# Kernel tuning notes

Hardware: AMD Instinct MI355X
Metric: run time of the kernel (lower is better)

The kernel has to match this reference:

```python
import jax, jax.numpy as jnp
import numpy as np
from jax.scipy.special import logsumexp

B, N, F_IN, HID = 8, 1024, 256, 128
RATIO = 0.5
NUM_LAYERS = 2
EPS_OT = 0.01  # forward default epsilon


def setup_inputs():
    key = jax.random.key(0)
    ks = jax.random.split(key, 6)
    x = jax.random.normal(ks[0], (B, N, F_IN), dtype=jnp.float32)
    adj = (jax.random.uniform(ks[1], (B, N, N)) < 0.02).astype(jnp.float32)
    adj = jnp.maximum(adj, jnp.swapaxes(adj, 1, 2))  # symmetric sparse-ish graph
    mask = jnp.ones((B, N), dtype=bool)
    W1 = jax.random.normal(ks[2], (F_IN, HID), dtype=jnp.float32) / np.sqrt(F_IN)
    b1 = jnp.zeros((HID,), dtype=jnp.float32)
    Watt = jax.random.normal(ks[3], (HID, 1), dtype=jnp.float32) / np.sqrt(HID)
    batt = jnp.zeros((1,), dtype=jnp.float32)
    W2 = jax.random.normal(ks[4], (HID, F_IN), dtype=jnp.float32) / np.sqrt(HID)
    b2 = jnp.zeros((F_IN,), dtype=jnp.float32)
    return dict(x=x, adj=adj, mask=mask, W1=W1, b1=b1, Watt=Watt, batt=batt,
                W2=W2, b2=b2, opt_epochs=20)


def _gcn_norm(adj):
    # DenseGCNConv add_loop + symmetric normalization
    n = adj.shape[-1]
    A = adj + jnp.eye(n, dtype=adj.dtype)
    d = jnp.maximum(A.sum(-1), 1.0) ** -0.5
    return d[..., :, None] * A * d[..., None, :]


def dense_gcn(x, adj, W, b, mask=None):
    out = jnp.einsum('bij,bjh->bih', _gcn_norm(adj), x @ W) + b
    if mask is not None:
        out = out * mask[..., None].astype(out.dtype)
    return out


def normalize_batch_adj(adj):
    # CoarsenBlock.normalize_batch_adj: self-loop sym-norm, zero-row masked
    n = adj.shape[-1]
    A = adj + jnp.eye(n, dtype=adj.dtype)
    d = jnp.maximum(A.sum(-1), 1.0) ** -0.5
    newA = d[..., :, None] * A * d[..., None, :]
    return (adj.sum(-1) > 0).astype(adj.dtype)[..., None] * newA


def coarsen_block(x, adj, Watt, batt):
    # attention score per node, squared then sigmoid  -> [B, N]
    alpha = jax.nn.sigmoid(dense_gcn(x, adj, Watt, batt) ** 2)[..., 0]
    norm_adj = normalize_batch_adj(adj)
    k = int(adj.shape[1] * RATIO) + 1
    cut = jax.lax.top_k(alpha, k)[0][:, -1]                 # per-sample k-th value
    cut_alpha = jax.nn.relu(alpha + 1e-7 - cut[:, None])    # soft top-k gate
    S = norm_adj * cut_alpha[:, None, :]
    S = S / jnp.maximum(jnp.abs(S).sum(-1, keepdims=True), 1e-12)  # row L1 norm
    emb = jnp.einsum('bij,bif->bjf', S, x)                  # S^T x
    tmp = jnp.einsum('bij,bik->bjk', S, adj)                # S^T adj
    new_adj = jnp.einsum('bjk,bkl->bjl', tmp, S)            # S^T adj S
    return emb, new_adj, S


def sinkhorn_loss(x, y, eps, niter):
    # squared-euclidean cost via gram trick (no [n,m,f] intermediate)
    C = (jnp.sum(x * x, -1)[:, None] + jnp.sum(y * y, -1)[None, :]
         - 2.0 * (x @ y.T))
    n, m = C.shape
    log_mu = jnp.full((n,), -np.log(n), dtype=C.dtype)
    log_nu = jnp.full((m,), -np.log(m), dtype=C.dtype)

    def M(u, v):
        return (-C + u[:, None] + v[None, :]) / eps

    def step(carry, _):
        u, v = carry
        u = eps * (log_mu - logsumexp(M(u, v), axis=1)) + u
        v = eps * (log_nu - logsumexp(M(u, v), axis=0)) + v
        return (u, v), None

    (u, v), _ = jax.lax.scan(step, (jnp.zeros_like(log_mu), jnp.zeros_like(log_nu)),
                             None, length=niter)
    pi = jnp.exp(M(u, v))
    return jnp.sum(pi * C)


def reference(x, adj, mask, W1, b1, Watt, batt, W2, b2, opt_epochs):
    x1 = jax.nn.relu(dense_gcn(x, adj, W1, b1, mask))
    xs0 = x1.mean(axis=1)
    new_adjs = [adj]
    Ss = []
    coarse_x, new_adj = x1, adj
    for _ in range(NUM_LAYERS):
        coarse_x, new_adj, S = coarsen_block(coarse_x, new_adj, Watt, batt)
        new_adjs.append(new_adj)
        Ss.append(S)
    x2 = dense_gcn(coarse_x, new_adj, W2, b2, mask)
    xs1 = x2.mean(axis=1)
    loss_fn = lambda a, b: sinkhorn_loss(a, b, EPS_OT, opt_epochs)
    opt_loss = jnp.sum(jax.vmap(loss_fn)(x, x2))
    return (xs0, xs1, new_adjs[0], new_adjs[1], new_adjs[2], Ss[0], Ss[1], opt_loss)
```

## Files before the change

kernel.cpp:

```cpp
#include <hip/hip_runtime.h>
#include <math.h>

#define BN   8
#define NN   1024
#define FIN  256
#define HIDN 128
#define KTOP 513
#define NITER 20
#define EPS_S 0.01f
#define INV_EPS 100.0f
#define LOG_MU (-6.9314718055994531f)
#define SNB 256

typedef __attribute__((ext_vector_type(8))) short bfrag8;
typedef __attribute__((ext_vector_type(4))) float facc4;

#define GLOAD16(g, l) __builtin_amdgcn_global_load_lds( \
    (const __attribute__((address_space(1))) unsigned int*)(g), \
    (__attribute__((address_space(3))) unsigned int*)(l), 16, 0, 0)

static __device__ __forceinline__ float wred_sum(float s) {
#pragma unroll
  for (int o = 32; o > 0; o >>= 1) s += __shfl_xor(s, o);
  return s;
}
static __device__ __forceinline__ unsigned short f2b(float f) {
  unsigned int u = __float_as_uint(f);
  u += 0x7fff + ((u >> 16) & 1);
  return (unsigned short)(u >> 16);
}
static __device__ __forceinline__ float b2f(unsigned short h) {
  return __uint_as_float((unsigned int)h << 16);
}

template<int WRBF, int WCOPY>
__global__ __launch_bounds__(256) void k_rowstats4(const float* __restrict__ adj,
                                                   float* __restrict__ dv,
                                                   float* __restrict__ rm,
                                                   unsigned short* __restrict__ abf,
                                                   float* __restrict__ ocopy) {
  int r0 = blockIdx.x << 2;
  int t = threadIdx.x, lane = t & 63, wv = t >> 6;
  __shared__ float sm[4][4];
#pragma unroll
  for (int r = 0; r < 4; ++r) {
    float4 v = ((const float4*)(adj + (long)(r0 + r) * NN))[t];
    if (WRBF) {
      ushort4 h; h.x = f2b(v.x); h.y = f2b(v.y); h.z = f2b(v.z); h.w = f2b(v.w);
      *(ushort4*)(abf + (long)(r0 + r) * NN + t * 4) = h;
    }
    if (WCOPY) ((float4*)(ocopy + (long)(r0 + r) * NN))[t] = v;
    float s = (v.x + v.y) + (v.z + v.w);
    s = wred_sum(s);
    if (lane == 0) sm[wv][r] = s;
  }
  __syncthreads();
  if (t < 4) {
    float tot = sm[0][t] + sm[1][t] + sm[2][t] + sm[3][t];
    dv[r0 + t] = rsqrtf(fmaxf(tot + 1.0f, 1.0f));
    rm[r0 + t] = tot > 0.0f ? 1.0f : 0.0f;
  }
}

__global__ __launch_bounds__(256) void k_f2b(const float* __restrict__ X,
                                             unsigned short* __restrict__ Y) {
  long i = ((long)blockIdx.x * 256 + threadIdx.x) * 4;
  float4 v = *(const float4*)(X + i);
  Y[i] = f2b(v.x); Y[i + 1] = f2b(v.y); Y[i + 2] = f2b(v.z); Y[i + 3] = f2b(v.w);
}

__global__ __launch_bounds__(256) void k_w1t(const float* __restrict__ W,
                                             unsigned short* __restrict__ Wt) {
  int idx = blockIdx.x * 256 + threadIdx.x;
  int n = idx >> 8, k = idx & 255;
  Wt[idx] = f2b(W[k * HIDN + n]);
}

__global__ __launch_bounds__(256) void k_split2(const float* __restrict__ X,
                                                unsigned short* __restrict__ Xh,
                                                unsigned short* __restrict__ Xl) {
  long i = ((long)blockIdx.x * 256 + threadIdx.x) * 4;
  float4 v = *(const float4*)(X + i);
  ushort4 h, l;
  h.x = f2b(v.x); l.x = f2b(v.x - b2f(h.x));
  h.y = f2b(v.y); l.y = f2b(v.y - b2f(h.y));
  h.z = f2b(v.z); l.z = f2b(v.z - b2f(h.z));
  h.w = f2b(v.w); l.w = f2b(v.w - b2f(h.w));
  *(ushort4*)(Xh + i) = h;
  *(ushort4*)(Xl + i) = l;
}

__global__ __launch_bounds__(256) void k_transp(const float* __restrict__ X,
                                                unsigned short* __restrict__ Xt,
                                                int R, int C) {
  __shared__ float tile[64][65];
  long bb = blockIdx.z;
  const float* Xb = X + bb * (long)R * C;
  unsigned short* Xtb = Xt + bb * (long)R * C;
  int r0 = blockIdx.y * 64, c0 = blockIdx.x * 64;
  int t = threadIdx.x;
  int tr = t >> 4, tc4 = (t & 15) * 4;
#pragma unroll
  for (int p = 0; p < 4; ++p) {
    float4 v = *(const float4*)(Xb + (long)(r0 + tr + p * 16) * C + c0 + tc4);
    tile[tr + p * 16][tc4 + 0] = v.x; tile[tr + p * 16][tc4 + 1] = v.y;
    tile[tr + p * 16][tc4 + 2] = v.z; tile[tr + p * 16][tc4 + 3] = v.w;
  }
  __syncthreads();
  int jj = t >> 2, i0 = (t & 3) * 16;
  unsigned short* orow = Xtb + (long)(c0 + jj) * R + r0 + i0;
#pragma unroll
  for (int q = 0; q < 16; ++q) orow[q] = f2b(tile[i0 + q][jj]);
}

template<int SPLIT>
__global__ __launch_bounds__(256) void k_stc(const float* __restrict__ XW,
                                             const float* __restrict__ dvv,
                                             unsigned short* __restrict__ Bh,
                                             unsigned short* __restrict__ Bl,
                                             int F) {
  __shared__ float tile[64][65];
  __shared__ float dl[64];
  int bz = blockIdx.z;
  const float* Xb = XW + (long)bz * NN * F;
  int j0 = blockIdx.x * 64;
  int n0 = blockIdx.y * 64;
  int t = threadIdx.x;
  int tr = t >> 4, tc4 = (t & 15) * 4;
#pragma unroll
  for (int p = 0; p < 4; ++p) {
    float4 v = *(const float4*)(Xb + (long)(j0 + tr + p * 16) * F + n0 + tc4);
    tile[tr + p * 16][tc4 + 0] = v.x; tile[tr + p * 16][tc4 + 1] = v.y;
    tile[tr + p * 16][tc4 + 2] = v.z; tile[tr + p * 16][tc4 + 3] = v.w;
  }
  if (t < 64) dl[t] = dvv[(bz << 10) + j0 + t];
  __syncthreads();
  int nn = t >> 2, i0 = (t & 3) * 16;
  long obase = ((long)bz * F + n0 + nn) * NN + j0 + i0;
#pragma unroll
  for (int q = 0; q < 16; ++q) {
    float v = tile[i0 + q][nn] * dl[i0 + q];
    unsigned short h = f2b(v);
    Bh[obase + q] = h;
    if (SPLIT) Bl[obase + q] = f2b(v - b2f(h));
  }
}

template<int WF32, int WBF>
__global__ __launch_bounds__(256) void k_mfma_nt(
    const unsigned short* __restrict__ A, const unsigned short* __restrict__ B,
    float* __restrict__ Cf, unsigned short* __restrict__ Cb,
    unsigned short* __restrict__ Cb2,
    int K, int ldA, int ldB, int ldC, long sA, long sB, long sC) {
  __shared__ unsigned short As[128 * 32];
  __shared__ unsigned short Bs[128 * 32];
  int bz = blockIdx.z;
  A += bz * sA; B += bz * sB;
  int m0 = blockIdx.y * 128, n0 = blockIdx.x * 128;
  int tid = threadIdx.x, lane = tid & 63, w = tid >> 6;
  int wr = w >> 1, wc = w & 1;
  facc4 acc[4][4];
#pragma unroll
  for (int i = 0; i < 4; ++i)
#pragma unroll
    for (int j = 0; j < 4; ++j)
#pragma unroll
      for (int q = 0; q < 4; ++q) acc[i][j][q] = 0.f;

  int rA0 = w * 16 + (lane >> 2);
  int kslot = lane & 3;

  for (int k0 = 0; k0 < K; k0 += 32) {
#pragma unroll
    for (int i = 0; i < 2; ++i) {
      int row = i * 64 + rA0;
      int ks = (kslot ^ (row & 3)) << 3;
      GLOAD16(A + (long)(m0 + row) * ldA + k0 + ks, As + (i * 64 + w * 16) * 32);
      GLOAD16(B + (long)(n0 + row) * ldB + k0 + ks, Bs + (i * 64 + w * 16) * 32);
    }
    __syncthreads();
    bfrag8 af[4], bfr[4];
#pragma unroll
    for (int mi = 0; mi < 4; ++mi) {
      int row = wr * 64 + mi * 16 + (lane & 15);
      int sl = (((lane >> 4) ^ (row & 3)) << 3);
      af[mi] = *(const bfrag8*)(As + row * 32 + sl);
    }
#pragma unroll
    for (int ni = 0; ni < 4; ++ni) {
      int row = wc * 64 + ni * 16 + (lane & 15);
      int sl = (((lane >> 4) ^ (row & 3)) << 3);
      bfr[ni] = *(const bfrag8*)(Bs + row * 32 + sl);
    }
#pragma unroll
    for (int mi = 0; mi < 4; ++mi)
#pragma unroll
      for (int ni = 0; ni < 4; ++ni)
        acc[mi][ni] = __builtin_amdgcn_mfma_f32_16x16x32_bf16(
            af[mi], bfr[ni], acc[mi][ni], 0, 0, 0);
    __syncthreads();
  }
  if (WF32) Cf += bz * sC;
  if (WBF) Cb += bz * sC;
  if (WBF == 2) Cb2 += bz * sC;
#pragma unroll
  for (int mi = 0; mi < 4; ++mi) {
    int rowb = m0 + wr * 64 + mi * 16 + ((lane >> 4) << 2);
#pragma unroll
    for (int ni = 0; ni < 4; ++ni) {
      int col = n0 + wc * 64 + ni * 16 + (lane & 15);
#pragma unroll
      for (int q = 0; q < 4; ++q) {
        long off = (long)(rowb + q) * ldC + col;
        float v = acc[mi][ni][q];
        if (WF32) Cf[off] = v;
        if (WBF == 1) Cb[off] = f2b(v);
        if (WBF == 2) {
          unsigned short h = f2b(v);
          Cb[off] = h;
          Cb2[off] = f2b(v - b2f(h));
        }
      }
    }
  }
}

template<int SPLIT, int RELU>
__global__ __launch_bounds__(256) void k_mfma_gcn(
    const unsigned short* __restrict__ Ah, const unsigned short* __restrict__ Al,
    const unsigned short* __restrict__ Bh, const unsigned short* __restrict__ Bl,
    const float* __restrict__ dvv, const float* __restrict__ XW,
    const float* __restrict__ bias, float* __restrict__ Cf, int F) {
  __shared__ unsigned short AsH[128 * 32], BsH[128 * 32];
  __shared__ unsigned short AsL[SPLIT ? 128 * 32 : 16], BsL[SPLIT ? 128 * 32 : 16];
  int bz = blockIdx.z;
  const unsigned short* Ahb = Ah + (long)bz * NN * NN;
  const unsigned short* Alb = SPLIT ? Al + (long)bz * NN * NN : nullptr;
  const unsigned short* Bhb = Bh + (long)bz * F * NN;
  const unsigned short* Blb = SPLIT ? Bl + (long)bz * F * NN : nullptr;
  int m0 = blockIdx.y * 128, n0 = blockIdx.x * 128;
  int tid = threadIdx.x, lane = tid & 63, w = tid >> 6;
  int wr = w >> 1, wc = w & 1;
  facc4 acc[4][4];
#pragma unroll
  for (int i = 0; i < 4; ++i)
#pragma unroll
    for (int j = 0; j < 4; ++j)
#pragma unroll
      for (int q = 0; q < 4; ++q) acc[i][j][q] = 0.f;

  int rA0 = w * 16 + (lane >> 2);
  int kslot = lane & 3;

  for (int k0 = 0; k0 < NN; k0 += 32) {
#pragma unroll
    for (int i = 0; i < 2; ++i) {
      int row = i * 64 + rA0;
      int ks = (kslot ^ (row & 3)) << 3;
      int ld = (i * 64 + w * 16) * 32;
      GLOAD16(Ahb + (long)(m0 + row) * NN + k0 + ks, AsH + ld);
      GLOAD16(Bhb + (long)(n0 + row) * NN + k0 + ks, BsH + ld);
      if (SPLIT) {
        GLOAD16(Alb + (long)(m0 + row) * NN + k0 + ks, AsL + ld);
        GLOAD16(Blb + (long)(n0 + row) * NN + k0 + ks, BsL + ld);
      }
    }
    __syncthreads();
    bfrag8 afh[4], bfh[4], afl[4], bfl[4];
#pragma unroll
    for (int mi = 0; mi < 4; ++mi) {
      int row = wr * 64 + mi * 16 + (lane & 15);
      int sl = (((lane >> 4) ^ (row & 3)) << 3);
      afh[mi] = *(const bfrag8*)(AsH + row * 32 + sl);
      if (SPLIT) afl[mi] = *(const bfrag8*)(AsL + row * 32 + sl);
    }
#pragma unroll
    for (int ni = 0; ni < 4; ++ni) {
      int row = wc * 64 + ni * 16 + (lane & 15);
      int sl = (((lane >> 4) ^ (row & 3)) << 3);
      bfh[ni] = *(const bfrag8*)(BsH + row * 32 + sl);
      if (SPLIT) bfl[ni] = *(const bfrag8*)(BsL + row * 32 + sl);
    }
#pragma unroll
    for (int mi = 0; mi < 4; ++mi)
#pragma unroll
      for (int ni = 0; ni < 4; ++ni) {
        acc[mi][ni] = __builtin_amdgcn_mfma_f32_16x16x32_bf16(
            afh[mi], bfh[ni], acc[mi][ni], 0, 0, 0);
        if (SPLIT) {
          acc[mi][ni] = __builtin_amdgcn_mfma_f32_16x16x32_bf16(
              afh[mi], bfl[ni], acc[mi][ni], 0, 0, 0);
          acc[mi][ni] = __builtin_amdgcn_mfma_f32_16x16x32_bf16(
              afl[mi], bfh[ni], acc[mi][ni], 0, 0, 0);
        }
      }
    __syncthreads();
  }
  Cf += (long)bz * NN * F;
#pragma unroll
  for (int mi = 0; mi < 4; ++mi) {
    int rowb = m0 + wr * 64 + mi * 16 + ((lane >> 4) << 2);
#pragma unroll
    for (int ni = 0; ni < 4; ++ni) {
      int col = n0 + wc * 64 + ni * 16 + (lane & 15);
      float bcol = bias[col];
#pragma unroll
      for (int q = 0; q < 4; ++q) {
        float dm = dvv[(bz << 10) + rowb + q];
        float xwv = XW[((long)(bz << 10) + rowb + q) * F + col];
        float v = dm * (acc[mi][ni][q] + dm * xwv) + bcol;
        if (RELU) v = fmaxf(v, 0.f);
        Cf[(long)(rowb + q) * F + col] = v;
      }
    }
  }
}

__global__ __launch_bounds__(256) void k_mfma_gram(
    const unsigned short* __restrict__ Ah, const unsigned short* __restrict__ Al,
    const unsigned short* __restrict__ Bh, const unsigned short* __restrict__ Bl,
    const float* __restrict__ xx, const float* __restrict__ yy,
    float* __restrict__ Cf, float* __restrict__ Ct) {
  __shared__ unsigned short AsH[128 * 32], AsL[128 * 32];
  __shared__ unsigned short BsH[128 * 32], BsL[128 * 32];
  int bz = blockIdx.z;
  long boff = (long)bz * NN * FIN;
  Ah += boff; Al += boff; Bh += boff; Bl += boff;
  const float* xxb = xx + (bz << 10);
  const float* yyb = yy + (bz << 10);
  int m0 = blockIdx.y * 128, n0 = blockIdx.x * 128;
  int tid = threadIdx.x, lane = tid & 63, w = tid >> 6;
  int wr = w >> 1, wc = w & 1;
  facc4 acc[4][4];
#pragma unroll
  for (int i = 0; i < 4; ++i)
#pragma unroll
    for (int j = 0; j < 4; ++j)
#pragma unroll
      for (int q = 0; q < 4; ++q) acc[i][j][q] = 0.f;

  int rA0 = w * 16 + (lane >> 2);
  int kslot = lane & 3;

  for (int k0 = 0; k0 < FIN; k0 += 32) {
#pragma unroll
    for (int i = 0; i < 2; ++i) {
      int row = i * 64 + rA0;
      int ks = (kslot ^ (row & 3)) << 3;
      long ga = (long)(m0 + row) * FIN + k0 + ks;
      long gb = (long)(n0 + row) * FIN + k0 + ks;
      int ld = (i * 64 + w * 16) * 32;
      GLOAD16(Ah + ga, AsH + ld);
      GLOAD16(Al + ga, AsL + ld);
      GLOAD16(Bh + gb, BsH + ld);
      GLOAD16(Bl + gb, BsL + ld);
    }
    __syncthreads();
    bfrag8 afh[4], afl[4], bfh[4], bfl[4];
#pragma unroll
    for (int mi = 0; mi < 4; ++mi) {
      int row = wr * 64 + mi * 16 + (lane & 15);
      int sl = (((lane >> 4) ^ (row & 3)) << 3);
      afh[mi] = *(const bfrag8*)(AsH + row * 32 + sl);
      afl[mi] = *(const bfrag8*)(AsL + row * 32 + sl);
    }
#pragma unroll
    for (int ni = 0; ni < 4; ++ni) {
      int row = wc * 64 + ni * 16 + (lane & 15);
      int sl = (((lane >> 4) ^ (row & 3)) << 3);
      bfh[ni] = *(const bfrag8*)(BsH + row * 32 + sl);
      bfl[ni] = *(const bfrag8*)(BsL + row * 32 + sl);
    }
#pragma unroll
    for (int mi = 0; mi < 4; ++mi)
#pragma unroll
      for (int ni = 0; ni < 4; ++ni) {
        acc[mi][ni] = __builtin_amdgcn_mfma_f32_16x16x32_bf16(
            afh[mi], bfh[ni], acc[mi][ni], 0, 0, 0);
        acc[mi][ni] = __builtin_amdgcn_mfma_f32_16x16x32_bf16(
            afh[mi], bfl[ni], acc[mi][ni], 0, 0, 0);
        acc[mi][ni] = __builtin_amdgcn_mfma_f32_16x16x32_bf16(
            afl[mi], bfh[ni], acc[mi][ni], 0, 0, 0);
      }
    __syncthreads();
  }
  Cf += (long)bz * NN * NN;
  Ct += (long)bz * NN * NN;
#pragma unroll
  for (int mi = 0; mi < 4; ++mi) {
    int rowb = m0 + wr * 64 + mi * 16 + ((lane >> 4) << 2);
#pragma unroll
    for (int ni = 0; ni < 4; ++ni) {
      int col = n0 + wc * 64 + ni * 16 + (lane & 15);
      float yv = yyb[col];
      float4 tv;
#pragma unroll
      for (int q = 0; q < 4; ++q) {
        float v = xxb[rowb + q] + yv - 2.f * acc[mi][ni][q];
        Cf[(long)(rowb + q) * NN + col] = v;
        ((float*)&tv)[q] = v;
      }
      *(float4*)(Ct + (long)col * NN + rowb) = tv;
    }
  }
}

__global__ __launch_bounds__(256) void k_rowdot(const float* __restrict__ X,
                                                const float* __restrict__ w,
                                                float* __restrict__ out) {
  int t = threadIdx.x; int lane = t & 63; int wv = t >> 6;
  int row = blockIdx.x * 4 + wv;
  const float* xr = X + (long)row * HIDN;
  float s = xr[lane] * w[lane] + xr[lane + 64] * w[lane + 64];
  s = wred_sum(s);
  if (lane == 0) out[row] = s;
}

__global__ __launch_bounds__(256) void k_alpha4(const float* __restrict__ adj,
                                                const float* __restrict__ dv,
                                                const float* __restrict__ s0,
                                                const float* __restrict__ batt,
                                                float* __restrict__ alpha) {
  int r0 = blockIdx.x << 2; int b = r0 >> 10; int i0 = r0 & (NN - 1);
  int t = threadIdx.x, lane = t & 63, wv = t >> 6;
  float4 d4 = ((const float4*)(dv + (b << 10)))[t];
  float4 s4 = ((const float4*)(s0 + (b << 10)))[t];
  float w4[4];
  w4[0] = d4.x * s4.x; w4[1] = d4.y * s4.y; w4[2] = d4.z * s4.z; w4[3] = d4.w * s4.w;
  __shared__ float sm[4][4];
#pragma unroll
  for (int r = 0; r < 4; ++r) {
    float4 a4 = ((const float4*)(adj + (long)(r0 + r) * NN))[t];
    float dot = a4.x * w4[0] + a4.y * w4[1] + a4.z * w4[2] + a4.w * w4[3];
    int i = i0 + r;
    if ((i >> 2) == t) dot += w4[i & 3];
    dot = wred_sum(dot);
    if (lane == 0) sm[wv][r] = dot;
  }
  __syncthreads();
  if (t < 4) {
    float dot = sm[0][t] + sm[1][t] + sm[2][t] + sm[3][t];
    float tt = dv[r0 + t] * dot + batt[0];
    alpha[r0 + t] = 1.f / (1.f + __expf(-tt * tt));
  }
}

__global__ __launch_bounds__(512) void k_topk(const float* __restrict__ alpha,
                                              float* __restrict__ cut) {
  __shared__ float smv[NN];
  int b = blockIdx.x; int t = threadIdx.x;
  smv[t] = alpha[(b << 10) + t];
  smv[t + 512] = alpha[(b << 10) + t + 512];
  __syncthreads();
  for (int k2 = 2; k2 <= NN; k2 <<= 1) {
    for (int j2 = k2 >> 1; j2 > 0; j2 >>= 1) {
      int i = ((t / j2) * (j2 << 1)) + (t % j2);
      int ixj = i + j2;
      bool up = ((i & k2) == 0);
      float a = smv[i], c = smv[ixj];
      if ((a > c) == up) { smv[i] = c; smv[ixj] = a; }
      __syncthreads();
    }
  }
  if (t == 0) cut[b] = smv[NN - KTOP];
}

__global__ __launch_bounds__(256) void k_sbuild4(const float* __restrict__ adj,
                                                 const float* __restrict__ dv,
                                                 const float* __restrict__ rm,
                                                 const float* __restrict__ alpha,
                                                 const float* __restrict__ cut,
                                                 float* __restrict__ S) {
  int r0 = blockIdx.x << 2; int b = r0 >> 10; int i0 = r0 & (NN - 1);
  int t = threadIdx.x, lane = t & 63, wv = t >> 6;
  float cb = cut[b];
  float4 d4 = ((const float4*)(dv + (b << 10)))[t];
  float4 al4 = ((const float4*)(alpha + (b << 10)))[t];
  float4 dg;
  dg.x = d4.x * fmaxf(al4.x + 1e-7f - cb, 0.f);
  dg.y = d4.y * fmaxf(al4.y + 1e-7f - cb, 0.f);
  dg.z = d4.z * fmaxf(al4.z + 1e-7f - cb, 0.f);
  dg.w = d4.w * fmaxf(al4.w + 1e-7f - cb, 0.f);
  __shared__ float sm[4][4];
  __shared__ float sinv[4];
  float4 vals[4];
#pragma unroll
  for (int r = 0; r < 4; ++r) {
    float di = dv[r0 + r] * rm[r0 + r];
    float4 a4 = ((const float4*)(adj + (long)(r0 + r) * NN))[t];
    int i = i0 + r;
    if ((i >> 2) == t) ((float*)&a4)[i & 3] += 1.f;
    vals[r].x = di * dg.x * a4.x; vals[r].y = di * dg.y * a4.y;
    vals[r].z = di * dg.z * a4.z; vals[r].w = di * dg.w * a4.w;
    float s = (fabsf(vals[r].x) + fabsf(vals[r].y)) +
              (fabsf(vals[r].z) + fabsf(vals[r].w));
    s = wred_sum(s);
    if (lane == 0) sm[wv][r] = s;
  }
  __syncthreads();
  if (t < 4) sinv[t] = 1.f / fmaxf(sm[0][t] + sm[1][t] + sm[2][t] + sm[3][t], 1e-12f);
  __syncthreads();
#pragma unroll
  for (int r = 0; r < 4; ++r) {
    float inv = sinv[r];
    float4 o; o.x = vals[r].x * inv; o.y = vals[r].y * inv;
    o.z = vals[r].z * inv; o.w = vals[r].w * inv;
    ((float4*)(S + (long)(r0 + r) * NN))[t] = o;
  }
}

template<int GCN>
__global__ __launch_bounds__(256) void k_gemm_ks(
    const float* __restrict__ A, const float* __restrict__ Bm, float* __restrict__ P,
    int M, int Nn, int K, int KS, long sA, long sB,
    const float* __restrict__ dv) {
  __shared__ float As[8][132];
  __shared__ float Bs[8][132];
  int z = blockIdx.z;
  int b = z / KS, ks = z % KS;
  int KC = K / KS;
  A += (long)b * sA; Bm += (long)b * sB;
  const float* dvb = GCN ? (dv + (long)b * NN) : nullptr;
  int m0 = blockIdx.y * 128, n0 = blockIdx.x * 128;
  int tid = threadIdx.x;
  int tx = tid & 15, ty = tid >> 4;
  float acc[8][8];
#pragma unroll
  for (int i = 0; i < 8; i++)
#pragma unroll
    for (int j = 0; j < 8; j++) acc[i][j] = 0.f;

  float drow = 0.f;
  if (GCN) drow = dvb[m0 + (tid >> 1)];

  for (int k0 = ks * KC; k0 < ks * KC + KC; k0 += 8) {
    {
      int r = tid >> 1, c4 = (tid & 1) * 4;
      float4 av = *(const float4*)(A + (long)(m0 + r) * K + k0 + c4);
      float a4[4] = {av.x, av.y, av.z, av.w};
      if (GCN) {
#pragma unroll
        for (int q = 0; q < 4; ++q) {
          int gj = k0 + c4 + q;
          float val = a4[q] + ((m0 + r) == gj ? 1.f : 0.f);
          a4[q] = drow * dvb[gj] * val;
        }
      }
      As[c4 + 0][r] = a4[0]; As[c4 + 1][r] = a4[1];
      As[c4 + 2][r] = a4[2]; As[c4 + 3][r] = a4[3];
    }
    {
      int kr = tid >> 5, c4 = (tid & 31) * 4;
      float4 bv = *(const float4*)(Bm + (long)(k0 + kr) * Nn + n0 + c4);
      *(float4*)&Bs[kr][c4] = bv;
    }
    __syncthreads();
#pragma unroll
    for (int k = 0; k < 8; ++k) {
      float av[8], bv[8];
      *(float4*)&av[0] = *(const float4*)&As[k][ty * 8];
      *(float4*)&av[4] = *(const float4*)&As[k][ty * 8 + 4];
      *(float4*)&bv[0] = *(const float4*)&Bs[k][tx * 8];
      *(float4*)&bv[4] = *(const float4*)&Bs[k][tx * 8 + 4];
#pragma unroll
      for (int i = 0; i < 8; i++)
#pragma unroll
        for (int j = 0; j < 8; j++)
          acc[i][j] = fmaf(av[i], bv[j], acc[i][j]);
    }
    __syncthreads();
  }
  float* Pz = P + (long)z * M * Nn;
#pragma unroll
  for (int i = 0; i < 8; ++i) {
    int m = m0 + ty * 8 + i;
    float* prow = Pz + (long)m * Nn + n0 + tx * 8;
    *(float4*)&prow[0] = *(float4*)&acc[i][0];
    *(float4*)&prow[4] = *(float4*)&acc[i][4];
  }
}

template<int RELU, int BIAS>
__global__ __launch_bounds__(256) void k_red_bias(
    const float* __restrict__ P, const float* __restrict__ bias,
    float* __restrict__ out, int Nn, int KS, long chunk) {
  long u = ((long)blockIdx.x * 256 + threadIdx.x) * 4;
  long b = u / chunk; long rem = u % chunk;
  const float* p = P + b * KS * chunk + rem;
  float4 s = *(const float4*)p;
  for (int k = 1; k < KS; ++k) {
    float4 q = *(const float4*)(p + (long)k * chunk);
    s.x += q.x; s.y += q.y; s.z += q.z; s.w += q.w;
  }
  if (BIAS) {
    int n = (int)(rem % Nn);
    s.x += bias[n]; s.y += bias[n + 1]; s.z += bias[n + 2]; s.w += bias[n + 3];
  }
  if (RELU) {
    s.x = fmaxf(s.x, 0.f); s.y = fmaxf(s.y, 0.f);
    s.z = fmaxf(s.z, 0.f); s.w = fmaxf(s.w, 0.f);
  }
  *(float4*)(out + u) = s;
}

__global__ __launch_bounds__(256) void k_colmean(const float* __restrict__ X, int Fd,
                                                 float* __restrict__ out) {
  int nb = Fd >> 6;
  int b = blockIdx.x / nb; int f0 = (blockIdx.x % nb) << 6;
  int t = threadIdx.x;
  int f = f0 + (t & 63); int rc = t >> 6;
  const float* xb = X + (long)b * NN * Fd;
  float s = 0.f;
  for (int i = rc * 256; i < rc * 256 + 256; ++i) s += xb[(long)i * Fd + f];
  __shared__ float sm[256];
  sm[t] = s; __syncthreads();
  if (t < 64) out[b * Fd + f] = (sm[t] + sm[t + 64] + sm[t + 128] + sm[t + 192]) * (1.f / NN);
}

__global__ __launch_bounds__(256) void k_sqnorm(const float* __restrict__ X, int Fd,
                                                float* __restrict__ out) {
  int t = threadIdx.x; int lane = t & 63; int wv = t >> 6;
  int row = blockIdx.x * 4 + wv;
  const float* xr = X + (long)row * Fd;
  float s = 0.f;
  for (int f = lane; f < Fd; f += 64) { float v = xr[f]; s = fmaf(v, v, s); }
  s = wred_sum(s);
  if (lane == 0) out[row] = s;
}


static __device__ __forceinline__ float4 load_cohere4(const float* p) {
  float4 v;
  asm volatile("global_load_dwordx4 %0, %1, off sc0 sc1\n\ts_waitcnt vmcnt(0)"
               : "=v"(v) : "v"(p) : "memory");
  return v;
}
static __device__ __forceinline__ float load_cohere1(const float* p) {
  float v;
  asm volatile("global_load_dword %0, %1, off sc0 sc1\n\ts_waitcnt vmcnt(0)"
               : "=v"(v) : "v"(p) : "memory");
  return v;
}
static __device__ __forceinline__ void store_cohere1(float* p, float v) {
  asm volatile("global_store_dword %0, %1, off sc0 sc1\n\ts_waitcnt vmcnt(0)"
               :: "v"(p), "v"(v) : "memory");
}

static __device__ __forceinline__ void stage_vec(float* __restrict__ vls,
                                                 const float* __restrict__ src,
                                                 int t) {
  if (t < 256) {
    float4 v = load_cohere4(src + t * 4);
    *(float4*)(vls + t * 4) = v;
  }
  __syncthreads();
}

static __device__ __forceinline__ void group_bar(int* __restrict__ slots,
                                                 int bid, int grp, int t, int g1) {
  __syncthreads();
  if (t == 0)
    __hip_atomic_store(&slots[bid * 16], g1, __ATOMIC_RELAXED,
                       __HIP_MEMORY_SCOPE_AGENT);
  if (t < 32) {
    int idx = ((grp << 5) + t) * 16;
    int spin = 0;
    while (__hip_atomic_load(&slots[idx], __ATOMIC_RELAXED,
                             __HIP_MEMORY_SCOPE_AGENT) < g1) {
      if (++spin > (1 << 20)) break;
      __builtin_amdgcn_s_sleep(1);
    }
  }
  __syncthreads();
}

template<int LOSS>
static __device__ __forceinline__ void pass_reg(const float4 (&Cr)[16],
    const float* __restrict__ vls, float* __restrict__ uout,
    int jc, int row, float* __restrict__ lossacc) {
  float mx = -3.0e38f;
#pragma unroll
  for (int k = 0; k < 16; ++k) {
    float4 v4 = *(const float4*)(vls + (k * 16 + jc) * 4);
    float ax = v4.x - Cr[k].x, ay = v4.y - Cr[k].y;
    float az = v4.z - Cr[k].z, aw = v4.w - Cr[k].w;
    mx = fmaxf(mx, fmaxf(fmaxf(ax, ay), fmaxf(az, aw)));
  }
#pragma unroll
  for (int m = 1; m <= 8; m <<= 1) mx = fmaxf(mx, __shfl_xor(mx, m));
  float ls = 0.f, ld = 0.f;
#pragma unroll
  for (int k = 0; k < 16; ++k) {
    float4 v4 = *(const float4*)(vls + (k * 16 + jc) * 4);
    float e;
    e = __expf(v4.x - Cr[k].x - mx); ls += e; if (LOSS) ld = fmaf(e, Cr[k].x, ld);
    e = __expf(v4.y - Cr[k].y - mx); ls += e; if (LOSS) ld = fmaf(e, Cr[k].y, ld);
    e = __expf(v4.z - Cr[k].z - mx); ls += e; if (LOSS) ld = fmaf(e, Cr[k].z, ld);
    e = __expf(v4.w - Cr[k].w - mx); ls += e; if (LOSS) ld = fmaf(e, Cr[k].w, ld);
  }
#pragma unroll
  for (int m = 1; m <= 8; m <<= 1) {
    ls += __shfl_xor(ls, m);
    if (LOSS) ld += __shfl_xor(ld, m);
  }
  if (jc == 0) {
    float uval = LOG_MU - (mx + __logf(ls));
    store_cohere1(uout + row, uval);
    if (LOSS) *lossacc += (ld / ls) * (1.0f / 1024.0f);
  }
}

__global__ __launch_bounds__(512, 2) void k_sink_reg(
    const float* __restrict__ Cm, const float* __restrict__ Ct,
    float* __restrict__ uvv, float* __restrict__ vvv,
    float* __restrict__ part, float* __restrict__ oloss,
    int* __restrict__ slots1, int* __restrict__ slots2) {
  int bid = blockIdx.x, t = threadIdx.x, lane = t & 63, wvi = t >> 6;
  int jc = lane & 15;
  int row = bid * 32 + wvi * 4 + (lane >> 4);
  int b = bid >> 5;
  __shared__ float vls[1024];
  float4 Creg[16], Ctreg[16];
  {
    const float4* cp = (const float4*)(Cm + (long)row * NN);
    const float4* tp = (const float4*)(Ct + (long)row * NN);
#pragma unroll
    for (int k = 0; k < 16; ++k) {
      float4 c = cp[k * 16 + jc], ct = tp[k * 16 + jc];
      Creg[k].x = c.x * INV_EPS;  Creg[k].y = c.y * INV_EPS;
      Creg[k].z = c.z * INV_EPS;  Creg[k].w = c.w * INV_EPS;
      Ctreg[k].x = ct.x * INV_EPS; Ctreg[k].y = ct.y * INV_EPS;
      Ctreg[k].z = ct.z * INV_EPS; Ctreg[k].w = ct.w * INV_EPS;
    }
  }
  const float* ub = uvv + (b << 10);
  const float* vb = vvv + (b << 10);
  float lossacc = 0.f;
  int g1 = 1;
  for (int it = 0; it < NITER; ++it) {
    stage_vec(vls, vb, t);
    pass_reg<0>(Creg, vls, uvv, jc, row, nullptr);
    group_bar(slots1, bid, b, t, g1); ++g1;
    stage_vec(vls, ub, t);
    if (it < NITER - 1) {
      pass_reg<0>(Ctreg, vls, vvv, jc, row, nullptr);
      group_bar(slots1, bid, b, t, g1); ++g1;
    } else {
      pass_reg<1>(Ctreg, vls, vvv, jc, row, &lossacc);
    }
  }
  float s = wred_sum(lossacc);
  __shared__ float lsm[8];
  if (lane == 0) lsm[wvi] = s;
  __syncthreads();
  if (t == 0) {
    float ps = 0.f;
#pragma unroll
    for (int i = 0; i < 8; ++i) ps += lsm[i];
    store_cohere1(part + bid, ps);
    __hip_atomic_store(&slots2[bid * 16], 1, __ATOMIC_RELAXED,
                       __HIP_MEMORY_SCOPE_AGENT);
  }
  if (bid == 0) {
    if (t < SNB) {
      int spin = 0;
      while (__hip_atomic_load(&slots2[t * 16], __ATOMIC_RELAXED,
                               __HIP_MEMORY_SCOPE_AGENT) < 1) {
        if (++spin > (1 << 20)) break;
        __builtin_amdgcn_s_sleep(1);
      }
    }
    __syncthreads();
    float s2 = 0.f;
    if (t < SNB) s2 = load_cohere1(part + t);
    s2 = wred_sum(s2);
    __shared__ float sm2[8];
    if (lane == 0) sm2[wvi] = s2;
    __syncthreads();
    if (t == 0) {
      float tot = 0.f;
#pragma unroll
      for (int i = 0; i < 8; ++i) tot += sm2[i];
      oloss[0] = tot * EPS_S;
    }
  }
}

extern "C" void kernel_launch(void* const* d_in, const int* in_sizes, int n_in,
                              void* d_out, int out_size, void* d_ws, size_t ws_size,
                              hipStream_t stream) {
  const float* x    = (const float*)d_in[0];
  const float* adj  = (const float*)d_in[1];
  const float* W1   = (const float*)d_in[3];
  const float* b1   = (const float*)d_in[4];
  const float* Watt = (const float*)d_in[5];
  const float* batt = (const float*)d_in[6];
  const float* W2   = (const float*)d_in[7];
  const float* b2   = (const float*)d_in[8];

  float* out = (float*)d_out;
  float* xs0   = out;
  float* xs1   = out + 1024;
  float* oadj0 = out + 3072;
  float* oadj1 = oadj0 + 8388608;
  float* oadj2 = oadj1 + 8388608;
  float* oS0   = oadj2 + 8388608;
  float* oS1   = oS0 + 8388608;
  float* oloss = oS1 + 8388608;

  float* ws   = (float*)d_ws;
  float* wXW  = ws;
  float* wCXA = wXW + 2097152;
  float* wCXB = wCXA + 1048576;
  float* wR   = wCXB + 1048576;
  float* wX2  = wR + 8388608;
  float* wStf = wX2 + 2097152;
  float* wCxtf= wStf + 4194304;
  float* wCt  = wCxtf + 524288;
  float* smb  = wCt + 8388608;

  unsigned short* tmp_bf = (unsigned short*)wR;
  unsigned short* a2h    = (unsigned short*)wCt;
  unsigned short* a2l    = a2h + 8388608;
  unsigned short* adj_bf = (unsigned short*)oadj2;
  unsigned short* St     = (unsigned short*)wStf;
  unsigned short* cxt    = (unsigned short*)wCxtf;
  unsigned short* x_bf   = (unsigned short*)wStf;
  unsigned short* Bg1    = (unsigned short*)wCxtf;
  unsigned short* Bg2h   = (unsigned short*)wStf;
  unsigned short* Bg2l   = (unsigned short*)(wStf + 2097152);
  unsigned short* xh  = (unsigned short*)wStf;
  unsigned short* xl  = xh + 2097152;
  unsigned short* x2h = xh + 4194304;
  unsigned short* x2l = xh + 6291456;
  float* Cmat = wR;
  float* d0 = smb;            float* rm0 = smb + 8192;
  float* d1 = smb + 16384;    float* rm1 = smb + 24576;
  float* d2 = smb + 32768;    float* rm2 = smb + 40960;
  float* s0v = smb + 49152;   float* alp = smb + 57344;
  float* xxv = smb + 65536;   float* yyv = smb + 73728;
  float* uv  = smb + 81920;   float* vv  = smb + 90112;
  float* cutv = smb + 98304;  float* part = smb + 98368;
  unsigned short* W1t = (unsigned short*)(smb + 98624);
  int* ibar = (int*)(smb + 115008);
  int* slots1 = ibar;
  int* slots2 = ibar + 4096;

  k_rowstats4<1, 1><<<2048, 256, 0, stream>>>(adj, d0, rm0, adj_bf, oadj0);

  k_f2b<<<2048, 256, 0, stream>>>(x, x_bf);
  k_w1t<<<128, 256, 0, stream>>>(W1, W1t);
  k_mfma_nt<1, 0><<<dim3(1, 64, 1), 256, 0, stream>>>(x_bf, W1t, wXW, nullptr,
      nullptr, 256, 256, 256, 128, 0L, 0L, 0L);
  k_stc<0><<<dim3(16, 2, 8), 256, 0, stream>>>(wXW, d0, Bg1, nullptr, HIDN);
  k_mfma_gcn<0, 1><<<dim3(1, 8, 8), 256, 0, stream>>>(adj_bf, nullptr, Bg1,
      nullptr, d0, wXW, b1, wCXA, HIDN);
  k_colmean<<<16, 256, 0, stream>>>(wCXA, HIDN, xs0);

  k_rowdot<<<2048, 256, 0, stream>>>(wCXA, Watt, s0v);
  k_alpha4<<<2048, 256, 0, stream>>>(adj, d0, s0v, batt, alp);
  k_topk<<<8, 512, 0, stream>>>(alp, cutv);
  k_sbuild4<<<2048, 256, 0, stream>>>(adj, d0, rm0, alp, cutv, oS0);
  k_transp<<<dim3(16, 16, 8), 256, 0, stream>>>(oS0, St, 1024, 1024);
  k_transp<<<dim3(2, 16, 8), 256, 0, stream>>>(wCXA, cxt, 1024, 128);
  k_mfma_nt<1, 0><<<dim3(1, 8, 8), 256, 0, stream>>>(St, cxt, wCXB, nullptr,
      nullptr, 1024, 1024, 1024, 128, 1048576L, 131072L, 131072L);
  k_mfma_nt<0, 1><<<dim3(8, 8, 8), 256, 0, stream>>>(St, adj_bf, nullptr, tmp_bf,
      nullptr, 1024, 1024, 1024, 1024, 1048576L, 1048576L, 1048576L);
  k_mfma_nt<1, 1><<<dim3(8, 8, 8), 256, 0, stream>>>(tmp_bf, St, oadj1, adj_bf,
      nullptr, 1024, 1024, 1024, 1024, 1048576L, 1048576L, 1048576L);
  k_rowstats4<0, 0><<<2048, 256, 0, stream>>>(oadj1, d1, rm1, nullptr, nullptr);

  k_rowdot<<<2048, 256, 0, stream>>>(wCXB, Watt, s0v);
  k_alpha4<<<2048, 256, 0, stream>>>(oadj1, d1, s0v, batt, alp);
  k_topk<<<8, 512, 0, stream>>>(alp, cutv);
  k_sbuild4<<<2048, 256, 0, stream>>>(oadj1, d1, rm1, alp, cutv, oS1);
  k_transp<<<dim3(16, 16, 8), 256, 0, stream>>>(oS1, St, 1024, 1024);
  k_transp<<<dim3(2, 16, 8), 256, 0, stream>>>(wCXB, cxt, 1024, 128);
  k_mfma_nt<1, 0><<<dim3(1, 8, 8), 256, 0, stream>>>(St, cxt, wCXA, nullptr,
      nullptr, 1024, 1024, 1024, 128, 1048576L, 131072L, 131072L);
  k_mfma_nt<0, 1><<<dim3(8, 8, 8), 256, 0, stream>>>(St, adj_bf, nullptr, tmp_bf,
      nullptr, 1024, 1024, 1024, 1024, 1048576L, 1048576L, 1048576L);
  k_mfma_nt<1, 2><<<dim3(8, 8, 8), 256, 0, stream>>>(tmp_bf, St, oadj2, a2h,
      a2l, 1024, 1024, 1024, 1024, 1048576L, 1048576L, 1048576L);
  k_rowstats4<0, 0><<<2048, 256, 0, stream>>>(oadj2, d2, rm2, nullptr, nullptr);

  k_gemm_ks<0><<<dim3(2, 64, 2), 256, 0, stream>>>(wCXA, W2, wR, 8192, FIN, HIDN,
      2, 0L, 0L, nullptr);
  k_red_bias<0, 0><<<2048, 256, 0, stream>>>(wR, nullptr, wXW, FIN, 2, 2097152L);
  k_stc<1><<<dim3(16, 4, 8), 256, 0, stream>>>(wXW, d2, Bg2h, Bg2l, FIN);
  k_mfma_gcn<1, 0><<<dim3(2, 8, 8), 256, 0, stream>>>(a2h, a2l, Bg2h, Bg2l,
      d2, wXW, b2, wX2, FIN);
  k_colmean<<<32, 256, 0, stream>>>(wX2, FIN, xs1);

  k_sqnorm<<<2048, 256, 0, stream>>>(x, FIN, xxv);
  k_sqnorm<<<2048, 256, 0, stream>>>(wX2, FIN, yyv);
  k_split2<<<2048, 256, 0, stream>>>(x, xh, xl);
  k_split2<<<2048, 256, 0, stream>>>(wX2, x2h, x2l);
  k_mfma_gram<<<dim3(8, 8, 8), 256, 0, stream>>>(xh, xl, x2h, x2l, xxv, yyv,
      Cmat, wCt);
  hipMemsetAsync(uv, 0, (size_t)2 * 8192 * 4, stream);
  hipMemsetAsync(ibar, 0, (size_t)8192 * 4, stream);
  k_sink_reg<<<SNB, 512, 0, stream>>>(Cmat, wCt, uv, vv, part, oloss,
                                      slots1, slots2);
}
```

Before: 749.3 us.

## Fuse coarsening GEMMs into one launch, fuse split with sqnorm, remap sinkhorn groups

```diff
diff --git a/kernel.cpp b/kernel.cpp
--- a/kernel.cpp
+++ b/kernel.cpp
@@ -76,18 +76,24 @@
   Wt[idx] = f2b(W[k * HIDN + n]);
 }
 
-__global__ __launch_bounds__(256) void k_split2(const float* __restrict__ X,
-                                                unsigned short* __restrict__ Xh,
-                                                unsigned short* __restrict__ Xl) {
-  long i = ((long)blockIdx.x * 256 + threadIdx.x) * 4;
-  float4 v = *(const float4*)(X + i);
+__global__ __launch_bounds__(256) void k_prep(const float* __restrict__ X,
+                                              unsigned short* __restrict__ Xh,
+                                              unsigned short* __restrict__ Xl,
+                                              float* __restrict__ sq) {
+  int t = threadIdx.x, lane = t & 63, wv = t >> 6;
+  int row = blockIdx.x * 4 + wv;
+  long base = (long)row * FIN + lane * 4;
+  float4 v = *(const float4*)(X + base);
   ushort4 h, l;
   h.x = f2b(v.x); l.x = f2b(v.x - b2f(h.x));
   h.y = f2b(v.y); l.y = f2b(v.y - b2f(h.y));
   h.z = f2b(v.z); l.z = f2b(v.z - b2f(h.z));
   h.w = f2b(v.w); l.w = f2b(v.w - b2f(h.w));
-  *(ushort4*)(Xh + i) = h;
-  *(ushort4*)(Xl + i) = l;
+  *(ushort4*)(Xh + base) = h;
+  *(ushort4*)(Xl + base) = l;
+  float s = v.x * v.x + v.y * v.y + v.z * v.z + v.w * v.w;
+  s = wred_sum(s);
+  if (lane == 0) sq[row] = s;
 }
 
 __global__ __launch_bounds__(256) void k_transp(const float* __restrict__ X,
@@ -220,6 +226,80 @@
           Cb[off] = h;
           Cb2[off] = f2b(v - b2f(h));
         }
+      }
+    }
+  }
+}
+
+__global__ __launch_bounds__(256) void k_coars(
+    const unsigned short* __restrict__ St, const unsigned short* __restrict__ Badj,
+    const unsigned short* __restrict__ cxt,
+    unsigned short* __restrict__ tmpo, float* __restrict__ embo) {
+  __shared__ unsigned short As[128 * 32];
+  __shared__ unsigned short Bs[128 * 32];
+  int bz = blockIdx.z;
+  int bx = blockIdx.x;
+  int em = (bx == 8);
+  const unsigned short* A = St + (long)bz * 1048576;
+  const unsigned short* B = em ? (cxt + (long)bz * 131072)
+                               : (Badj + (long)bz * 1048576);
+  int m0 = blockIdx.y * 128, n0 = em ? 0 : bx * 128;
+  int tid = threadIdx.x, lane = tid & 63, w = tid >> 6;
+  int wr = w >> 1, wc = w & 1;
+  facc4 acc[4][4];
+#pragma unroll
+  for (int i = 0; i < 4; ++i)
+#pragma unroll
+    for (int j = 0; j < 4; ++j)
+#pragma unroll
+      for (int q = 0; q < 4; ++q) acc[i][j][q] = 0.f;
+
+  int rA0 = w * 16 + (lane >> 2);
+  int kslot = lane & 3;
+
+  for (int k0 = 0; k0 < NN; k0 += 32) {
+#pragma unroll
+    for (int i = 0; i < 2; ++i) {
+      int row = i * 64 + rA0;
+      int ks = (kslot ^ (row & 3)) << 3;
+      GLOAD16(A + (long)(m0 + row) * NN + k0 + ks, As + (i * 64 + w * 16) * 32);
+      GLOAD16(B + (long)(n0 + row) * NN + k0 + ks, Bs + (i * 64 + w * 16) * 32);
+    }
+    __syncthreads();
+    bfrag8 af[4], bfr[4];
+#pragma unroll
+    for (int mi = 0; mi < 4; ++mi) {
+      int row = wr * 64 + mi * 16 + (lane & 15);
+      int sl = (((lane >> 4) ^ (row & 3)) << 3);
+      af[mi] = *(const bfrag8*)(As + row * 32 + sl);
+    }
+#pragma unroll
+    for (int ni = 0; ni < 4; ++ni) {
+      int row = wc * 64 + ni * 16 + (lane & 15);
+      int sl = (((lane >> 4) ^ (row & 3)) << 3);
+      bfr[ni] = *(const bfrag8*)(Bs + row * 32 + sl);
+    }
+#pragma unroll
+    for (int mi = 0; mi < 4; ++mi)
+#pragma unroll
+      for (int ni = 0; ni < 4; ++ni)
+        acc[mi][ni] = __builtin_amdgcn_mfma_f32_16x16x32_bf16(
+            af[mi], bfr[ni], acc[mi][ni], 0, 0, 0);
+    __syncthreads();
+  }
+#pragma unroll
+  for (int mi = 0; mi < 4; ++mi) {
+    int rowb = m0 + wr * 64 + mi * 16 + ((lane >> 4) << 2);
+#pragma unroll
+    for (int ni = 0; ni < 4; ++ni) {
+      int col = n0 + wc * 64 + ni * 16 + (lane & 15);
+#pragma unroll
+      for (int q = 0; q < 4; ++q) {
+        float v = acc[mi][ni][q];
+        if (em)
+          embo[(long)bz * 131072 + (long)(rowb + q) * HIDN + col] = v;
+        else
+          tmpo[(long)bz * 1048576 + (long)(rowb + q) * NN + col] = f2b(v);
       }
     }
   }
@@ -617,17 +697,6 @@
   if (t < 64) out[b * Fd + f] = (sm[t] + sm[t + 64] + sm[t + 128] + sm[t + 192]) * (1.f / NN);
 }
 
-__global__ __launch_bounds__(256) void k_sqnorm(const float* __restrict__ X, int Fd,
-                                                float* __restrict__ out) {
-  int t = threadIdx.x; int lane = t & 63; int wv = t >> 6;
-  int row = blockIdx.x * 4 + wv;
-  const float* xr = X + (long)row * Fd;
-  float s = 0.f;
-  for (int f = lane; f < Fd; f += 64) { float v = xr[f]; s = fmaf(v, v, s); }
-  s = wred_sum(s);
-  if (lane == 0) out[row] = s;
-}
-
 
 static __device__ __forceinline__ float4 load_cohere4(const float* p) {
   float4 v;
@@ -663,7 +732,7 @@
     __hip_atomic_store(&slots[bid * 16], g1, __ATOMIC_RELAXED,
                        __HIP_MEMORY_SCOPE_AGENT);
   if (t < 32) {
-    int idx = ((grp << 5) + t) * 16;
+    int idx = ((t << 3) + grp) * 16;
     int spin = 0;
     while (__hip_atomic_load(&slots[idx], __ATOMIC_RELAXED,
                              __HIP_MEMORY_SCOPE_AGENT) < g1) {
@@ -678,12 +747,15 @@
 static __device__ __forceinline__ void pass_reg(const float4 (&Cr)[16],
     const float* __restrict__ vls, float* __restrict__ uout,
     int jc, int row, float* __restrict__ lossacc) {
+  float4 vr[16];
+#pragma unroll
+  for (int k = 0; k < 16; ++k)
+    vr[k] = *(const float4*)(vls + (k * 16 + jc) * 4);
   float mx = -3.0e38f;
 #pragma unroll
   for (int k = 0; k < 16; ++k) {
-    float4 v4 = *(const float4*)(vls + (k * 16 + jc) * 4);
-    float ax = v4.x - Cr[k].x, ay = v4.y - Cr[k].y;
-    float az = v4.z - Cr[k].z, aw = v4.w - Cr[k].w;
+    float ax = vr[k].x - Cr[k].x, ay = vr[k].y - Cr[k].y;
+    float az = vr[k].z - Cr[k].z, aw = vr[k].w - Cr[k].w;
     mx = fmaxf(mx, fmaxf(fmaxf(ax, ay), fmaxf(az, aw)));
   }
 #pragma unroll
@@ -691,12 +763,11 @@
   float ls = 0.f, ld = 0.f;
 #pragma unroll
   for (int k = 0; k < 16; ++k) {
-    float4 v4 = *(const float4*)(vls + (k * 16 + jc) * 4);
     float e;
-    e = __expf(v4.x - Cr[k].x - mx); ls += e; if (LOSS) ld = fmaf(e, Cr[k].x, ld);
-    e = __expf(v4.y - Cr[k].y - mx); ls += e; if (LOSS) ld = fmaf(e, Cr[k].y, ld);
-    e = __expf(v4.z - Cr[k].z - mx); ls += e; if (LOSS) ld = fmaf(e, Cr[k].z, ld);
-    e = __expf(v4.w - Cr[k].w - mx); ls += e; if (LOSS) ld = fmaf(e, Cr[k].w, ld);
+    e = __expf(vr[k].x - Cr[k].x - mx); ls += e; if (LOSS) ld = fmaf(e, Cr[k].x, ld);
+    e = __expf(vr[k].y - Cr[k].y - mx); ls += e; if (LOSS) ld = fmaf(e, Cr[k].y, ld);
+    e = __expf(vr[k].z - Cr[k].z - mx); ls += e; if (LOSS) ld = fmaf(e, Cr[k].z, ld);
+    e = __expf(vr[k].w - Cr[k].w - mx); ls += e; if (LOSS) ld = fmaf(e, Cr[k].w, ld);
   }
 #pragma unroll
   for (int m = 1; m <= 8; m <<= 1) {
@@ -717,8 +788,9 @@
     int* __restrict__ slots1, int* __restrict__ slots2) {
   int bid = blockIdx.x, t = threadIdx.x, lane = t & 63, wvi = t >> 6;
   int jc = lane & 15;
-  int row = bid * 32 + wvi * 4 + (lane >> 4);
-  int b = bid >> 5;
+  int grp = bid & 7;
+  int inner = bid >> 3;
+  int row = (grp << 10) + inner * 32 + wvi * 4 + (lane >> 4);
   __shared__ float vls[1024];
   float4 Creg[16], Ctreg[16];
   {
@@ -733,18 +805,18 @@
       Ctreg[k].z = ct.z * INV_EPS; Ctreg[k].w = ct.w * INV_EPS;
     }
   }
-  const float* ub = uvv + (b << 10);
-  const float* vb = vvv + (b << 10);
+  const float* ub = uvv + (grp << 10);
+  const float* vb = vvv + (grp << 10);
   float lossacc = 0.f;
   int g1 = 1;
   for (int it = 0; it < NITER; ++it) {
     stage_vec(vls, vb, t);
     pass_reg<0>(Creg, vls, uvv, jc, row, nullptr);
-    group_bar(slots1, bid, b, t, g1); ++g1;
+    group_bar(slots1, bid, grp, t, g1); ++g1;
     stage_vec(vls, ub, t);
     if (it < NITER - 1) {
       pass_reg<0>(Ctreg, vls, vvv, jc, row, nullptr);
-      group_bar(slots1, bid, b, t, g1); ++g1;
+      group_bar(slots1, bid, grp, t, g1); ++g1;
     } else {
       pass_reg<1>(Ctreg, vls, vvv, jc, row, &lossacc);
     }
@@ -863,10 +935,7 @@
   k_sbuild4<<<2048, 256, 0, stream>>>(adj, d0, rm0, alp, cutv, oS0);
   k_transp<<<dim3(16, 16, 8), 256, 0, stream>>>(oS0, St, 1024, 1024);
   k_transp<<<dim3(2, 16, 8), 256, 0, stream>>>(wCXA, cxt, 1024, 128);
-  k_mfma_nt<1, 0><<<dim3(1, 8, 8), 256, 0, stream>>>(St, cxt, wCXB, nullptr,
-      nullptr, 1024, 1024, 1024, 128, 1048576L, 131072L, 131072L);
-  k_mfma_nt<0, 1><<<dim3(8, 8, 8), 256, 0, stream>>>(St, adj_bf, nullptr, tmp_bf,
-      nullptr, 1024, 1024, 1024, 1024, 1048576L, 1048576L, 1048576L);
+  k_coars<<<dim3(9, 8, 8), 256, 0, stream>>>(St, adj_bf, cxt, tmp_bf, wCXB);
   k_mfma_nt<1, 1><<<dim3(8, 8, 8), 256, 0, stream>>>(tmp_bf, St, oadj1, adj_bf,
       nullptr, 1024, 1024, 1024, 1024, 1048576L, 1048576L, 1048576L);
   k_rowstats4<0, 0><<<2048, 256, 0, stream>>>(oadj1, d1, rm1, nullptr, nullptr);
@@ -877,10 +946,7 @@
   k_sbuild4<<<2048, 256, 0, stream>>>(oadj1, d1, rm1, alp, cutv, oS1);
   k_transp<<<dim3(16, 16, 8), 256, 0, stream>>>(oS1, St, 1024, 1024);
   k_transp<<<dim3(2, 16, 8), 256, 0, stream>>>(wCXB, cxt, 1024, 128);
-  k_mfma_nt<1, 0><<<dim3(1, 8, 8), 256, 0, stream>>>(St, cxt, wCXA, nullptr,
-      nullptr, 1024, 1024, 1024, 128, 1048576L, 131072L, 131072L);
-  k_mfma_nt<0, 1><<<dim3(8, 8, 8), 256, 0, stream>>>(St, adj_bf, nullptr, tmp_bf,
-      nullptr, 1024, 1024, 1024, 1024, 1048576L, 1048576L, 1048576L);
+  k_coars<<<dim3(9, 8, 8), 256, 0, stream>>>(St, adj_bf, cxt, tmp_bf, wCXA);
   k_mfma_nt<1, 2><<<dim3(8, 8, 8), 256, 0, stream>>>(tmp_bf, St, oadj2, a2h,
       a2l, 1024, 1024, 1024, 1024, 1048576L, 1048576L, 1048576L);
   k_rowstats4<0, 0><<<2048, 256, 0, stream>>>(oadj2, d2, rm2, nullptr, nullptr);
@@ -893,10 +959,8 @@
       d2, wXW, b2, wX2, FIN);
   k_colmean<<<32, 256, 0, stream>>>(wX2, FIN, xs1);
 
-  k_sqnorm<<<2048, 256, 0, stream>>>(x, FIN, xxv);
-  k_sqnorm<<<2048, 256, 0, stream>>>(wX2, FIN, yyv);
-  k_split2<<<2048, 256, 0, stream>>>(x, xh, xl);
-  k_split2<<<2048, 256, 0, stream>>>(wX2, x2h, x2l);
+  k_prep<<<2048, 256, 0, stream>>>(x, xh, xl, xxv);
+  k_prep<<<2048, 256, 0, stream>>>(wX2, x2h, x2l, yyv);
   k_mfma_gram<<<dim3(8, 8, 8), 256, 0, stream>>>(xh, xl, x2h, x2l, xxv, yyv,
       Cmat, wCt);
   hipMemsetAsync(uv, 0, (size_t)2 * 8192 * 4, stream);
```

Result: no change. 743.3 us (-0.8%).
